# Performance work log

Hardware: AMD Instinct MI355X
Metric: run time of the kernel (lower is better)

## Reference

```python
import jax, jax.numpy as jnp
import numpy as np

B, S, D_MODEL, D_K, D_V = 4, 2048, 1024, 1024, 1024


def setup_inputs() -> dict:
    key = jax.random.key(0)
    k1, k2, k3, k4 = jax.random.split(key, 4)
    scale = 1.0 / np.sqrt(D_MODEL)
    x = jax.random.normal(k1, (B, S, D_MODEL), dtype=jnp.float32)
    Wq = jax.random.normal(k2, (D_K, D_MODEL), dtype=jnp.float32) * scale
    Wk = jax.random.normal(k3, (D_K, D_MODEL), dtype=jnp.float32) * scale
    Wv = jax.random.normal(k4, (D_V, D_MODEL), dtype=jnp.float32) * scale
    # causal mask: position i may attend to j <= i (True = keep)
    mask = jnp.broadcast_to(jnp.tril(jnp.ones((S, S), dtype=bool)), (B, S, S))
    return {"x": x, "mask": mask, "Wq": Wq, "Wk": Wk, "Wv": Wv}


def reference(x, mask, Wq, Wk, Wv):
    # nn.Linear(d, k, bias=False): y = x @ W.T with W of shape [k, d]
    q = jnp.einsum('bsd,kd->bsk', x, Wq)
    k = jnp.einsum('bsd,kd->bsk', x, Wk)
    v = jnp.einsum('bsd,vd->bsv', x, Wv)
    scores = jnp.einsum('bik,bjk->bij', q, k) / jnp.sqrt(jnp.float32(D_K))
    s = jnp.where(mask, scores, -jnp.inf)
    # masked, fully-masked-row-safe softmax (fully masked rows -> all zeros,
    # matching softmax[all-masked rows] = 0 in the original)
    m = jnp.max(s, axis=-1, keepdims=True)
    m_safe = jnp.where(jnp.isfinite(m), m, 0.0)
    e = jnp.exp(s - m_safe)          # exp(-inf) = 0 for masked entries
    denom = jnp.sum(e, axis=-1, keepdims=True)
    p = e / jnp.where(denom == 0.0, 1.0, denom)
    return jnp.einsum('bij,bjv->biv', p, v)
```

## Files before the change

### kernel.cpp

```cpp
#include <hip/hip_runtime.h>
#include <hip/hip_bf16.h>
#include <stdint.h>

#define SEQ   2048
#define DM    1024
#define NBAT  4

typedef __attribute__((ext_vector_type(8))) short  short8;
typedef __attribute__((ext_vector_type(4))) float  floatx4;

__device__ __forceinline__ unsigned short f2b(float f) {
    __hip_bfloat16 h = __float2bfloat16(f);
    unsigned short r;
    __builtin_memcpy(&r, &h, 2);
    return r;
}

__device__ __forceinline__ ushort4 pack4(float a, float b, float c, float d) {
    ushort4 u; u.x = f2b(a); u.y = f2b(b); u.z = f2b(c); u.w = f2b(d); return u;
}

__device__ __forceinline__ void gload16(const void* g, void* s) {
    __builtin_amdgcn_global_load_lds(
        (const __attribute__((address_space(1))) unsigned int*)(uintptr_t)g,
        (__attribute__((address_space(3))) unsigned int*)(uintptr_t)s,
        16, 0, 0);
}

__global__ void prep(const float4* __restrict__ x,
                     const float4* __restrict__ w0, const float4* __restrict__ w1,
                     const float4* __restrict__ w2,
                     ushort4* __restrict__ xb, ushort4* __restrict__ wall,
                     float* __restrict__ rsum)
{
    const int b = blockIdx.x;
    const int t = threadIdx.x;
    if (b < 8192) {
        const int i = b * 256 + t;
        float4 f = x[i];
        xb[i] = pack4(f.x, f.y, f.z, f.w);
    } else if (b < 11264) {
        const int idx  = b - 8192;
        const int wsel = idx >> 10;
        const int i    = (idx & 1023) * 256 + t;
        const float4* src = (wsel == 0) ? w0 : (wsel == 1) ? w1 : w2;
        float4 f = src[i];
        wall[(size_t)wsel * 262144 + i] = pack4(f.x, f.y, f.z, f.w);
    } else {
        rsum[(b - 11264) * 256 + t] = 0.f;
    }
}

#define SLOT 12288

__global__ __launch_bounds__(512, 2) void qkv_gemm(
    const unsigned short* __restrict__ A, const unsigned short* __restrict__ Bm,
    unsigned short* __restrict__ Qo, unsigned short* __restrict__ Ko,
    unsigned short* __restrict__ Vto, float qscale)
{
    __shared__ __align__(16) unsigned short lds[5 * SLOT];

    const int bid = blockIdx.x;
    const int wg  = (bid & 7) * 96 + (bid >> 3);
    const int mt  = wg / 24, nt = wg - mt * 24;
    const int m0  = mt * 256, n0 = nt * 128;

    const int t    = threadIdx.x;
    const int w    = t >> 6;
    const int lane = t & 63;
    const int wr   = w >> 1, wc = w & 1;
    const int r    = lane & 15, q = lane >> 4;

    const int rp      = (r & ~1) | ((r ^ (r >> 1)) & 1);
    const int fr      = (r & 3) ^ ((r >> 2) & 3);
    const int laneOff = rp * 32 + ((q ^ fr) << 3);

    const int R   = t >> 2;
    const int sR  = (R & ~1) | ((R ^ (R >> 1)) & 1);
    const int fS  = (sR & 3) ^ ((sR >> 2) & 3);
    const int jS  = ((t & 3) ^ fS) << 3;
    const int wS  = w * 512;

    floatx4 acc[4][4];
#pragma unroll
    for (int i = 0; i < 4; i++)
#pragma unroll
        for (int j = 0; j < 4; j++)
            acc[i][j] = (floatx4){0.f, 0.f, 0.f, 0.f};

#define STG3(T4, DSTS) do { \
    const int kb_ = ((T4) < 32) ? (T4) * 32 : 0; \
    gload16(A  + (((size_t)(m0 +       sR)) << 10) + kb_ + jS, &lds[(DSTS) +        wS]); \
    gload16(A  + (((size_t)(m0 + 128 + sR)) << 10) + kb_ + jS, &lds[(DSTS) + 4096 + wS]); \
    gload16(Bm + (((size_t)(n0 +       sR)) << 10) + kb_ + jS, &lds[(DSTS) + 8192 + wS]); \
  } while (0)

    STG3(0, 0 * SLOT);
    STG3(1, 1 * SLOT);
    STG3(2, 2 * SLOT);
    STG3(3, 3 * SLOT);
    asm volatile("s_waitcnt vmcnt(9)" ::: "memory");
    __builtin_amdgcn_s_barrier();

    int p = 0, q4 = 4;
    for (int tt = 0; tt < 32; ++tt) {
        const int slotS = p * SLOT;
        const int aBase = slotS + wr * 4096 + laneOff;
        const int aB = slotS + (wr >> 1) * 4096 + (wr & 1) * 2048 + laneOff;
        const int bB = slotS + 8192 + wc * 2048 + laneOff;
        (void)aBase;

        short8 af0 = *(const short8*)&lds[aB +    0];
        short8 af1 = *(const short8*)&lds[aB +  512];
        short8 af2 = *(const short8*)&lds[aB + 1024];
        short8 af3 = *(const short8*)&lds[aB + 1536];
        short8 bf0 = *(const short8*)&lds[bB +    0];
        short8 bf1 = *(const short8*)&lds[bB +  512];
        short8 bf2 = *(const short8*)&lds[bB + 1024];
        short8 bf3 = *(const short8*)&lds[bB + 1536];

        STG3(tt + 4, q4 * SLOT);

        asm volatile("s_waitcnt vmcnt(9)" ::: "memory");
        __builtin_amdgcn_s_barrier();
        asm volatile("s_waitcnt lgkmcnt(0)" ::: "memory");
        __builtin_amdgcn_s_setprio(1);
        acc[0][0] = __builtin_amdgcn_mfma_f32_16x16x32_bf16(af0, bf0, acc[0][0], 0, 0, 0);
        acc[0][1] = __builtin_amdgcn_mfma_f32_16x16x32_bf16(af0, bf1, acc[0][1], 0, 0, 0);
        acc[0][2] = __builtin_amdgcn_mfma_f32_16x16x32_bf16(af0, bf2, acc[0][2], 0, 0, 0);
        acc[0][3] = __builtin_amdgcn_mfma_f32_16x16x32_bf16(af0, bf3, acc[0][3], 0, 0, 0);
        acc[1][0] = __builtin_amdgcn_mfma_f32_16x16x32_bf16(af1, bf0, acc[1][0], 0, 0, 0);
        acc[1][1] = __builtin_amdgcn_mfma_f32_16x16x32_bf16(af1, bf1, acc[1][1], 0, 0, 0);
        acc[1][2] = __builtin_amdgcn_mfma_f32_16x16x32_bf16(af1, bf2, acc[1][2], 0, 0, 0);
        acc[1][3] = __builtin_amdgcn_mfma_f32_16x16x32_bf16(af1, bf3, acc[1][3], 0, 0, 0);
        acc[2][0] = __builtin_amdgcn_mfma_f32_16x16x32_bf16(af2, bf0, acc[2][0], 0, 0, 0);
        acc[2][1] = __builtin_amdgcn_mfma_f32_16x16x32_bf16(af2, bf1, acc[2][1], 0, 0, 0);
        acc[2][2] = __builtin_amdgcn_mfma_f32_16x16x32_bf16(af2, bf2, acc[2][2], 0, 0, 0);
        acc[2][3] = __builtin_amdgcn_mfma_f32_16x16x32_bf16(af2, bf3, acc[2][3], 0, 0, 0);
        acc[3][0] = __builtin_amdgcn_mfma_f32_16x16x32_bf16(af3, bf0, acc[3][0], 0, 0, 0);
        acc[3][1] = __builtin_amdgcn_mfma_f32_16x16x32_bf16(af3, bf1, acc[3][1], 0, 0, 0);
        acc[3][2] = __builtin_amdgcn_mfma_f32_16x16x32_bf16(af3, bf2, acc[3][2], 0, 0, 0);
        acc[3][3] = __builtin_amdgcn_mfma_f32_16x16x32_bf16(af3, bf3, acc[3][3], 0, 0, 0);
        __builtin_amdgcn_s_setprio(0);
        __builtin_amdgcn_s_barrier();

        p  = (p  == 4) ? 0 : p  + 1;
        q4 = (q4 == 4) ? 0 : q4 + 1;
    }
#undef STG3

    const int gmb = m0 + wr * 64 + q * 4;
    const int gnb = n0 + wc * 64 + r;
    if (nt < 8) {
#pragma unroll
        for (int i = 0; i < 4; i++) {
            const int gm = gmb + i * 16;
#pragma unroll
            for (int j = 0; j < 4; j++) {
                const int gn = gnb + j * 16;
#pragma unroll
                for (int rr = 0; rr < 4; rr++)
                    Qo[(size_t)(gm + rr) * 1024 + gn] = f2b(acc[i][j][rr] * qscale);
            }
        }
    } else if (nt < 16) {
#pragma unroll
        for (int i = 0; i < 4; i++) {
            const int gm = gmb + i * 16;
#pragma unroll
            for (int j = 0; j < 4; j++) {
                const int gn = gnb + j * 16;
#pragma unroll
                for (int rr = 0; rr < 4; rr++)
                    Ko[(size_t)(gm + rr) * 1024 + (gn - 1024)] = f2b(acc[i][j][rr]);
            }
        }
    } else {
#pragma unroll
        for (int i = 0; i < 4; i++) {
            const int gm = gmb + i * 16;
            const int b  = gm >> 11;
            const int s  = gm & 2047;
#pragma unroll
            for (int j = 0; j < 4; j++) {
                const int v = gnb + j * 16 - 2048;
                *(ushort4*)&Vto[((size_t)(b * 1024 + v)) * 2048 + s] =
                    pack4(acc[i][j][0], acc[i][j][1], acc[i][j][2], acc[i][j][3]);
            }
        }
    }
}

template<int MODE>
__global__ __launch_bounds__(256) void attn64(
    const unsigned short* __restrict__ Ag, const unsigned short* __restrict__ Bg,
    void* __restrict__ Cv, float* __restrict__ rowsum)
{
    const int z = blockIdx.z;
    int m0, n0;
    if (MODE == 0) {
        const int f = blockIdx.x;
        int ti = (int)((sqrtf(4.f * f + 1.f) - 1.f) * 0.5f);
        while ((ti + 1) * (ti + 2) <= f) ti++;
        while (ti * (ti + 1) > f) ti--;
        const int tj = f - ti * (ti + 1);
        m0 = ti * 128;
        n0 = tj * 64;
    } else {
        m0 = (int)(gridDim.y - 1 - blockIdx.y) * 128;
        n0 = blockIdx.x * 64;
    }

    const int lda = (MODE == 0) ? DM : SEQ;
    const int ldb = (MODE == 0) ? DM : SEQ;
    const unsigned short* A  = Ag + (size_t)z * ((MODE == 0) ? SEQ * DM : SEQ * SEQ);
    const unsigned short* Bm = Bg + (size_t)z * ((MODE == 0) ? SEQ * DM : DM * SEQ);
    const int kEnd = (MODE == 0) ? DM : (m0 + 128);

    __shared__ __align__(16) unsigned short As[128 * 64];
    __shared__ __align__(16) unsigned short Bs[64 * 64];

    const int t    = threadIdx.x;
    const int w    = t >> 6;
    const int lane = t & 63;
    const int r    = lane & 15, q = lane >> 4;

    floatx4 acc[2][4];
#pragma unroll
    for (int i = 0; i < 2; i++)
#pragma unroll
        for (int j = 0; j < 4; j++)
            acc[i][j] = (floatx4){0.f, 0.f, 0.f, 0.f};

    const int rr0 = t >> 3;
    const int pg  = (t & 7) ^ ((t >> 3) & 7);
    const int swz = r & 7;

    for (int k0 = 0; k0 < kEnd; k0 += 64) {
        const size_t ka = (size_t)k0 + pg * 8;
#pragma unroll
        for (int g = 0; g < 4; g++)
            gload16(A + (size_t)(m0 + g * 32 + rr0) * lda + ka,
                    As + g * 2048 + (size_t)w * 512);
#pragma unroll
        for (int g = 0; g < 2; g++)
            gload16(Bm + (size_t)(n0 + g * 32 + rr0) * ldb + ka,
                    Bs + g * 2048 + (size_t)w * 512);
        __builtin_amdgcn_s_waitcnt(0);
        __syncthreads();

#pragma unroll
        for (int kk = 0; kk < 2; kk++) {
            short8 af[2], bf[4];
            const int slot = ((kk * 4 + q) ^ swz) * 8;
#pragma unroll
            for (int i = 0; i < 2; i++)
                af[i] = *(const short8*)&As[(w * 32 + i * 16 + r) * 64 + slot];
#pragma unroll
            for (int j = 0; j < 4; j++)
                bf[j] = *(const short8*)&Bs[(j * 16 + r) * 64 + slot];
#pragma unroll
            for (int i = 0; i < 2; i++)
#pragma unroll
                for (int j = 0; j < 4; j++)
                    acc[i][j] = __builtin_amdgcn_mfma_f32_16x16x32_bf16(bf[j], af[i], acc[i][j], 0, 0, 0);
        }
        __syncthreads();
    }

    const int gmb = m0 + w * 32 + r;
    const int gnb = n0 + q * 4;
    if (MODE == 0) {
        unsigned short* E = (unsigned short*)Cv + (size_t)z * SEQ * SEQ;
        float* rs = rowsum + (size_t)z * SEQ;
#pragma unroll
        for (int i = 0; i < 2; i++) {
            const int gm = gmb + i * 16;
            float part = 0.f;
#pragma unroll
            for (int j = 0; j < 4; j++) {
                const int gn = gnb + j * 16;
                float e0 = (gn + 0 <= gm) ? __expf(acc[i][j][0]) : 0.f;
                float e1 = (gn + 1 <= gm) ? __expf(acc[i][j][1]) : 0.f;
                float e2 = (gn + 2 <= gm) ? __expf(acc[i][j][2]) : 0.f;
                float e3 = (gn + 3 <= gm) ? __expf(acc[i][j][3]) : 0.f;
                part += (e0 + e1) + (e2 + e3);
                *(ushort4*)&E[(size_t)gm * SEQ + gn] = pack4(e0, e1, e2, e3);
            }
            part += __shfl_xor(part, 16, 64);
            part += __shfl_xor(part, 32, 64);
            if (q == 0) atomicAdd(&rs[gm], part);
        }
    } else {
        float* C = (float*)Cv + (size_t)z * SEQ * DM;
        const float* rs = rowsum + (size_t)z * SEQ;
#pragma unroll
        for (int i = 0; i < 2; i++) {
            const int gm = gmb + i * 16;
            const float inv = 1.0f / rs[gm];
#pragma unroll
            for (int j = 0; j < 4; j++) {
                const int gn = gnb + j * 16;
                float4 o;
                o.x = acc[i][j][0] * inv;
                o.y = acc[i][j][1] * inv;
                o.z = acc[i][j][2] * inv;
                o.w = acc[i][j][3] * inv;
                *(float4*)&C[(size_t)gm * DM + gn] = o;
            }
        }
    }
}

extern "C" void kernel_launch(void* const* d_in, const int* in_sizes, int n_in,
                              void* d_out, int out_size, void* d_ws, size_t ws_size,
                              hipStream_t stream) {
    (void)in_sizes; (void)n_in; (void)out_size; (void)ws_size;
    const float* x  = (const float*)d_in[0];
    const float* Wq = (const float*)d_in[2];
    const float* Wk = (const float*)d_in[3];
    const float* Wv = (const float*)d_in[4];

    char* base = (char*)d_ws;
    size_t off = 0;
    auto alloc = [&](size_t n) { char* p = base + off; off += (n + 255) & ~(size_t)255; return p; };

    unsigned short* xb   = (unsigned short*)alloc((size_t)NBAT * SEQ * DM * 2);
    unsigned short* wall = (unsigned short*)alloc((size_t)3 * DM * DM * 2);
    unsigned short* Qb   = (unsigned short*)alloc((size_t)NBAT * SEQ * DM * 2);
    unsigned short* Kb   = (unsigned short*)alloc((size_t)NBAT * SEQ * DM * 2);
    unsigned short* Vtb  = (unsigned short*)alloc((size_t)NBAT * DM * SEQ * 2);
    unsigned short* E    = (unsigned short*)alloc((size_t)NBAT * SEQ * SEQ * 2);
    float*          rsum = (float*)alloc((size_t)NBAT * SEQ * 4);

    const dim3 blk(256);

    prep<<<dim3(11296), blk, 0, stream>>>(
        (const float4*)x, (const float4*)Wq, (const float4*)Wk, (const float4*)Wv,
        (ushort4*)xb, (ushort4*)wall, rsum);

    qkv_gemm<<<dim3(768), dim3(512), 0, stream>>>(
        xb, wall, Qb, Kb, Vtb, 0.03125f);

    attn64<0><<<dim3(272, 1, NBAT), blk, 0, stream>>>(Qb, Kb, E, rsum);

    attn64<1><<<dim3(DM / 64, SEQ / 128, NBAT), blk, 0, stream>>>(E, Vtb, d_out, rsum);
}
```

Measured before the change: 280.8 us.

## Restage QKV GEMM with 64-wide K tiles in a triple-buffered LDS ring

The QKV projection GEMM now stages 64-element K slices per pipeline step in three LDS slots, replacing five 32-wide slots. Each slice is consumed in two 32-wide MFMA half-steps, and the A and B global-to-LDS loads are split across those halves. The LDS layout moves to 64-element rows with an XOR swizzle on 16-byte chunks. The aim is to halve the number of pipeline iterations and keep the load issue spread out while using larger, more coalesced row loads. In exchange the prefetch is shallower (two stages ahead instead of four), and there are still two barriers per half-step.

```diff
diff --git a/kernel.cpp b/kernel.cpp
--- a/kernel.cpp
+++ b/kernel.cpp
@@ -51,14 +51,14 @@
     }
 }
 
-#define SLOT 12288
+#define SLOTS 24576
 
 __global__ __launch_bounds__(512, 2) void qkv_gemm(
     const unsigned short* __restrict__ A, const unsigned short* __restrict__ Bm,
     unsigned short* __restrict__ Qo, unsigned short* __restrict__ Ko,
     unsigned short* __restrict__ Vto, float qscale)
 {
-    __shared__ __align__(16) unsigned short lds[5 * SLOT];
+    __shared__ __align__(16) unsigned short lds[3 * SLOTS];
 
     const int bid = blockIdx.x;
     const int wg  = (bid & 7) * 96 + (bid >> 3);
@@ -71,15 +71,13 @@
     const int wr   = w >> 1, wc = w & 1;
     const int r    = lane & 15, q = lane >> 4;
 
-    const int rp      = (r & ~1) | ((r ^ (r >> 1)) & 1);
-    const int fr      = (r & 3) ^ ((r >> 2) & 3);
-    const int laneOff = rp * 32 + ((q ^ fr) << 3);
-
-    const int R   = t >> 2;
-    const int sR  = (R & ~1) | ((R ^ (R >> 1)) & 1);
-    const int fS  = (sR & 3) ^ ((sR >> 2) & 3);
-    const int jS  = ((t & 3) ^ fS) << 3;
-    const int wS  = w * 512;
+    const int srow = lane >> 3;
+    const int scol = ((lane & 7) ^ srow) << 3;
+
+    const int aoff = (wr >> 1) * 8192 + ((wr & 1) * 64 + r) * 64;
+    const int boff = 16384 + (wc * 64 + r) * 64;
+    const int sk0  = ((0 + q) ^ (r & 7)) * 8;
+    const int sk1  = ((4 + q) ^ (r & 7)) * 8;
 
     floatx4 acc[4][4];
 #pragma unroll
@@ -88,66 +86,93 @@
         for (int j = 0; j < 4; j++)
             acc[i][j] = (floatx4){0.f, 0.f, 0.f, 0.f};
 
-#define STG3(T4, DSTS) do { \
-    const int kb_ = ((T4) < 32) ? (T4) * 32 : 0; \
-    gload16(A  + (((size_t)(m0 +       sR)) << 10) + kb_ + jS, &lds[(DSTS) +        wS]); \
-    gload16(A  + (((size_t)(m0 + 128 + sR)) << 10) + kb_ + jS, &lds[(DSTS) + 4096 + wS]); \
-    gload16(Bm + (((size_t)(n0 +       sR)) << 10) + kb_ + jS, &lds[(DSTS) + 8192 + wS]); \
+#define STGA(KB, SL) do { \
+    gload16(A + (((size_t)(m0 +       w * 16 + srow)) << 10) + (KB) + scol, &lds[(SL) +         w * 1024]); \
+    gload16(A + (((size_t)(m0 +   8 + w * 16 + srow)) << 10) + (KB) + scol, &lds[(SL) +         w * 1024 + 512]); \
+    gload16(A + (((size_t)(m0 + 128 + w * 16 + srow)) << 10) + (KB) + scol, &lds[(SL) + 8192 +  w * 1024]); \
+    gload16(A + (((size_t)(m0 + 136 + w * 16 + srow)) << 10) + (KB) + scol, &lds[(SL) + 8192 +  w * 1024 + 512]); \
   } while (0)
-
-    STG3(0, 0 * SLOT);
-    STG3(1, 1 * SLOT);
-    STG3(2, 2 * SLOT);
-    STG3(3, 3 * SLOT);
-    asm volatile("s_waitcnt vmcnt(9)" ::: "memory");
+#define STGB(KB, SL) do { \
+    gload16(Bm + (((size_t)(n0 +      w * 16 + srow)) << 10) + (KB) + scol, &lds[(SL) + 16384 + w * 1024]); \
+    gload16(Bm + (((size_t)(n0 +  8 + w * 16 + srow)) << 10) + (KB) + scol, &lds[(SL) + 16384 + w * 1024 + 512]); \
+  } while (0)
+
+#define MFMA16() do { \
+    acc[0][0] = __builtin_amdgcn_mfma_f32_16x16x32_bf16(af0, bf0, acc[0][0], 0, 0, 0); \
+    acc[0][1] = __builtin_amdgcn_mfma_f32_16x16x32_bf16(af0, bf1, acc[0][1], 0, 0, 0); \
+    acc[0][2] = __builtin_amdgcn_mfma_f32_16x16x32_bf16(af0, bf2, acc[0][2], 0, 0, 0); \
+    acc[0][3] = __builtin_amdgcn_mfma_f32_16x16x32_bf16(af0, bf3, acc[0][3], 0, 0, 0); \
+    acc[1][0] = __builtin_amdgcn_mfma_f32_16x16x32_bf16(af1, bf0, acc[1][0], 0, 0, 0); \
+    acc[1][1] = __builtin_amdgcn_mfma_f32_16x16x32_bf16(af1, bf1, acc[1][1], 0, 0, 0); \
+    acc[1][2] = __builtin_amdgcn_mfma_f32_16x16x32_bf16(af1, bf2, acc[1][2], 0, 0, 0); \
+    acc[1][3] = __builtin_amdgcn_mfma_f32_16x16x32_bf16(af1, bf3, acc[1][3], 0, 0, 0); \
+    acc[2][0] = __builtin_amdgcn_mfma_f32_16x16x32_bf16(af2, bf0, acc[2][0], 0, 0, 0); \
+    acc[2][1] = __builtin_amdgcn_mfma_f32_16x16x32_bf16(af2, bf1, acc[2][1], 0, 0, 0); \
+    acc[2][2] = __builtin_amdgcn_mfma_f32_16x16x32_bf16(af2, bf2, acc[2][2], 0, 0, 0); \
+    acc[2][3] = __builtin_amdgcn_mfma_f32_16x16x32_bf16(af2, bf3, acc[2][3], 0, 0, 0); \
+    acc[3][0] = __builtin_amdgcn_mfma_f32_16x16x32_bf16(af3, bf0, acc[3][0], 0, 0, 0); \
+    acc[3][1] = __builtin_amdgcn_mfma_f32_16x16x32_bf16(af3, bf1, acc[3][1], 0, 0, 0); \
+    acc[3][2] = __builtin_amdgcn_mfma_f32_16x16x32_bf16(af3, bf2, acc[3][2], 0, 0, 0); \
+    acc[3][3] = __builtin_amdgcn_mfma_f32_16x16x32_bf16(af3, bf3, acc[3][3], 0, 0, 0); \
+  } while (0)
+
+    STGA(0, 0);
+    STGB(0, 0);
+    STGA(64, SLOTS);
+    STGB(64, SLOTS);
+    asm volatile("s_waitcnt vmcnt(6)" ::: "memory");
     __builtin_amdgcn_s_barrier();
 
-    int p = 0, q4 = 4;
-    for (int tt = 0; tt < 32; ++tt) {
-        const int slotS = p * SLOT;
-        const int aBase = slotS + wr * 4096 + laneOff;
-        const int aB = slotS + (wr >> 1) * 4096 + (wr & 1) * 2048 + laneOff;
-        const int bB = slotS + 8192 + wc * 2048 + laneOff;
-        (void)aBase;
-
-        short8 af0 = *(const short8*)&lds[aB +    0];
-        short8 af1 = *(const short8*)&lds[aB +  512];
-        short8 af2 = *(const short8*)&lds[aB + 1024];
-        short8 af3 = *(const short8*)&lds[aB + 1536];
-        short8 bf0 = *(const short8*)&lds[bB +    0];
-        short8 bf1 = *(const short8*)&lds[bB +  512];
-        short8 bf2 = *(const short8*)&lds[bB + 1024];
-        short8 bf3 = *(const short8*)&lds[bB + 1536];
-
-        STG3(tt + 4, q4 * SLOT);
-
-        asm volatile("s_waitcnt vmcnt(9)" ::: "memory");
-        __builtin_amdgcn_s_barrier();
-        asm volatile("s_waitcnt lgkmcnt(0)" ::: "memory");
-        __builtin_amdgcn_s_setprio(1);
-        acc[0][0] = __builtin_amdgcn_mfma_f32_16x16x32_bf16(af0, bf0, acc[0][0], 0, 0, 0);
-        acc[0][1] = __builtin_amdgcn_mfma_f32_16x16x32_bf16(af0, bf1, acc[0][1], 0, 0, 0);
-        acc[0][2] = __builtin_amdgcn_mfma_f32_16x16x32_bf16(af0, bf2, acc[0][2], 0, 0, 0);
-        acc[0][3] = __builtin_amdgcn_mfma_f32_16x16x32_bf16(af0, bf3, acc[0][3], 0, 0, 0);
-        acc[1][0] = __builtin_amdgcn_mfma_f32_16x16x32_bf16(af1, bf0, acc[1][0], 0, 0, 0);
-        acc[1][1] = __builtin_amdgcn_mfma_f32_16x16x32_bf16(af1, bf1, acc[1][1], 0, 0, 0);
-        acc[1][2] = __builtin_amdgcn_mfma_f32_16x16x32_bf16(af1, bf2, acc[1][2], 0, 0, 0);
-        acc[1][3] = __builtin_amdgcn_mfma_f32_16x16x32_bf16(af1, bf3, acc[1][3], 0, 0, 0);
-        acc[2][0] = __builtin_amdgcn_mfma_f32_16x16x32_bf16(af2, bf0, acc[2][0], 0, 0, 0);
-        acc[2][1] = __builtin_amdgcn_mfma_f32_16x16x32_bf16(af2, bf1, acc[2][1], 0, 0, 0);
-        acc[2][2] = __builtin_amdgcn_mfma_f32_16x16x32_bf16(af2, bf2, acc[2][2], 0, 0, 0);
-        acc[2][3] = __builtin_amdgcn_mfma_f32_16x16x32_bf16(af2, bf3, acc[2][3], 0, 0, 0);
-        acc[3][0] = __builtin_amdgcn_mfma_f32_16x16x32_bf16(af3, bf0, acc[3][0], 0, 0, 0);
-        acc[3][1] = __builtin_amdgcn_mfma_f32_16x16x32_bf16(af3, bf1, acc[3][1], 0, 0, 0);
-        acc[3][2] = __builtin_amdgcn_mfma_f32_16x16x32_bf16(af3, bf2, acc[3][2], 0, 0, 0);
-        acc[3][3] = __builtin_amdgcn_mfma_f32_16x16x32_bf16(af3, bf3, acc[3][3], 0, 0, 0);
-        __builtin_amdgcn_s_setprio(0);
-        __builtin_amdgcn_s_barrier();
-
-        p  = (p  == 4) ? 0 : p  + 1;
-        q4 = (q4 == 4) ? 0 : q4 + 1;
-    }
-#undef STG3
+    short8 af0, af1, af2, af3, bf0, bf1, bf2, bf3;
+
+    for (int tt = 0; tt < 16; ++tt) {
+        const int sl  = (tt % 3) * SLOTS;
+        const int nsl = ((tt + 2) % 3) * SLOTS;
+        const int nkb = (tt + 2 < 16) ? (tt + 2) * 64 : 0;
+
+        {
+            const int aB = sl + aoff + sk0;
+            const int bB = sl + boff + sk0;
+            af0 = *(const short8*)&lds[aB +    0];
+            af1 = *(const short8*)&lds[aB + 1024];
+            af2 = *(const short8*)&lds[aB + 2048];
+            af3 = *(const short8*)&lds[aB + 3072];
+            bf0 = *(const short8*)&lds[bB +    0];
+            bf1 = *(const short8*)&lds[bB + 1024];
+            bf2 = *(const short8*)&lds[bB + 2048];
+            bf3 = *(const short8*)&lds[bB + 3072];
+            STGA(nkb, nsl);
+            __builtin_amdgcn_s_barrier();
+            asm volatile("s_waitcnt lgkmcnt(0)" ::: "memory");
+            __builtin_amdgcn_s_setprio(1);
+            MFMA16();
+            __builtin_amdgcn_s_setprio(0);
+            __builtin_amdgcn_s_barrier();
+        }
+        {
+            const int aB = sl + aoff + sk1;
+            const int bB = sl + boff + sk1;
+            af0 = *(const short8*)&lds[aB +    0];
+            af1 = *(const short8*)&lds[aB + 1024];
+            af2 = *(const short8*)&lds[aB + 2048];
+            af3 = *(const short8*)&lds[aB + 3072];
+            bf0 = *(const short8*)&lds[bB +    0];
+            bf1 = *(const short8*)&lds[bB + 1024];
+            bf2 = *(const short8*)&lds[bB + 2048];
+            bf3 = *(const short8*)&lds[bB + 3072];
+            STGB(nkb, nsl);
+            asm volatile("s_waitcnt vmcnt(6)" ::: "memory");
+            __builtin_amdgcn_s_barrier();
+            asm volatile("s_waitcnt lgkmcnt(0)" ::: "memory");
+            __builtin_amdgcn_s_setprio(1);
+            MFMA16();
+            __builtin_amdgcn_s_setprio(0);
+            __builtin_amdgcn_s_barrier();
+        }
+    }
+#undef STGA
+#undef STGB
+#undef MFMA16
 
     const int gmb = m0 + wr * 64 + q * 4;
     const int gnb = n0 + wc * 64 + r;
```

Result: faster. 267.4 us (-4.8%).
